# Kernel tuning notes

Measured on AMD Instinct MI355X. Metric: run time of the kernel, lower is better.

The kernel has to match this reference:

```python
import jax, jax.numpy as jnp
import numpy as np

LOSS_WEIGHT = 1.0


def setup_inputs() -> dict:
    key = jax.random.key(0)
    k1, k2 = jax.random.split(key)
    pred = jax.random.normal(k1, (4, 8192, 3), dtype=jnp.float32)
    target = jax.random.normal(k2, (4, 8192, 3), dtype=jnp.float32)
    return {"pred": pred, "target": target}


def _chamfer(pred, target):
    # pred: [B, N, 3], target: [B, M, 3]
    # squared pairwise distances d2[b, n, m] = ||pred[b,n] - target[b,m]||^2
    x2 = jnp.sum(pred * pred, axis=-1)            # [B, N]
    y2 = jnp.sum(target * target, axis=-1)        # [B, M]
    xy = jnp.einsum('bnd,bmd->bnm', pred, target)  # [B, N, M]
    d2 = x2[:, :, None] + y2[:, None, :] - 2.0 * xy
    d2 = jnp.maximum(d2, 0.0)  # numerical floor
    # bidirectional nearest-neighbor distances
    cham_x = jnp.min(d2, axis=2)  # [B, N] pred -> target
    cham_y = jnp.min(d2, axis=1)  # [B, M] target -> pred
    # point_reduction='mean' then batch_reduction='mean'
    loss = jnp.mean(cham_x, axis=1).mean() + jnp.mean(cham_y, axis=1).mean()
    return LOSS_WEIGHT * loss


def reference(pred, target):
    return _chamfer(pred, target)
```

## Files before the change

kernel.cpp:

```cpp
#include <hip/hip_runtime.h>

#define BATCH 4
#define NPTS 8192
#define PTOT (BATCH * NPTS)
#define NJH 8
#define TILES (NPTS / 32 / NJH)

typedef __attribute__((ext_vector_type(8))) short short8;
typedef __attribute__((ext_vector_type(16))) float f32x16;

__device__ __forceinline__ ushort f2bf(float f) {
    unsigned u = __float_as_uint(f);
    unsigned r = (u + 0x7fffu + ((u >> 16) & 1u)) >> 16;
    return (ushort)r;
}
__device__ __forceinline__ float bf2f(ushort b) {
    return __uint_as_float(((unsigned)b) << 16);
}

__device__ __forceinline__ float tree16(const f32x16 a, float run) {
    float m0 = fminf(fminf(a[0],  a[1]),  a[2]);
    float m1 = fminf(fminf(a[3],  a[4]),  a[5]);
    float m2 = fminf(fminf(a[6],  a[7]),  a[8]);
    float m3 = fminf(fminf(a[9],  a[10]), a[11]);
    float m4 = fminf(fminf(a[12], a[13]), a[14]);
    float n0 = fminf(fminf(m0, m1), m2);
    float n1 = fminf(fminf(m3, m4), a[15]);
    return fminf(run, fminf(n0, n1));
}

__global__ __launch_bounds__(256) void pack_k(const float* __restrict__ pred,
                                              const float* __restrict__ tgt,
                                              ushort* __restrict__ Qpan,
                                              ushort* __restrict__ Rpan) {
    int i = blockIdx.x * 256 + threadIdx.x;
    int cloud = (i >= PTOT) ? 1 : 0;
    int jg = cloud ? i - PTOT : i;
    const float* s = cloud ? tgt : pred;
    float c0 = s[3 * jg + 0], c1 = s[3 * jg + 1], c2 = s[3 * jg + 2];
    float c[3] = {c0, c1, c2};
    ushort hh[3], ll[3], mh[3], ml[3];
#pragma unroll
    for (int d = 0; d < 3; ++d) {
        ushort h = f2bf(c[d]); float hf = bf2f(h);
        ushort l = f2bf(c[d] - hf); float lf = bf2f(l);
        hh[d] = h; ll[d] = l;
        mh[d] = f2bf(-2.0f * hf);
        ml[d] = f2bf(-2.0f * lf);
    }
    float n2 = fmaf(c0, c0, fmaf(c1, c1, c2 * c2));
    ushort n2h = f2bf(n2);
    ushort n2l = f2bf(n2 - bf2f(n2h));
    const ushort ONE = 0x3F80;

    __attribute__((aligned(16))) ushort a[16] = {
        hh[0], hh[1], hh[2], ll[0], ll[1], ll[2], n2h, n2l,
        hh[0], hh[1], hh[2], ll[0], ll[1], ll[2], ONE, ONE};
    __attribute__((aligned(16))) ushort blo[8] = {
        mh[0], mh[1], mh[2], mh[0], mh[1], mh[2], ONE, ONE};
    __attribute__((aligned(16))) ushort bhi[8] = {
        ml[0], ml[1], ml[2], ml[0], ml[1], ml[2], n2h, n2l};

    ushort* ad = Qpan + (size_t)i * 16;
    *(uint4*)ad       = *(const uint4*)a;
    *(uint4*)(ad + 8) = *(const uint4*)(a + 8);

    int loc = jg & (NPTS - 1);
    int t   = loc >> 5;
    int col = loc & 31;
    size_t bb = ((size_t)cloud * PTOT + (size_t)(jg >> 13) * NPTS) * 16
              + (size_t)t * 512 + (size_t)col * 8;
    *(uint4*)(Rpan + bb)       = *(const uint4*)blo;
    *(uint4*)(Rpan + bb + 256) = *(const uint4*)bhi;
}

__global__ __launch_bounds__(512, 4) void chamfer_mfma_k(const ushort* __restrict__ Qpan,
                                                         const ushort* __restrict__ Rpan,
                                                         float* __restrict__ part) {
    __shared__ ushort Rsm[TILES * 512];

    int bid  = blockIdx.x;
    int qblk = bid & 15;
    int b    = (bid >> 4) & 3;
    int dir  = (bid >> 6) & 1;
    int jh   = bid >> 7;
    int tid  = threadIdx.x;
    int lane = tid & 63;
    int wave = tid >> 6;

    const ushort* Qp = Qpan + ((size_t)dir * PTOT + (size_t)b * NPTS) * 16;
    const ushort* Rp = Rpan + ((size_t)(1 - dir) * PTOT + (size_t)b * NPTS) * 16
                            + (size_t)jh * TILES * 512;

    {
        const float4* src = (const float4*)Rp;
        float4* dst = (float4*)Rsm;
#pragma unroll
        for (int it = 0; it < 4; ++it)
            dst[it * 512 + tid] = src[it * 512 + tid];
    }

    int q = qblk * 512 + wave * 64;
    const short8 qf0 = *reinterpret_cast<const short8*>(
        Qp + (size_t)(q + (lane & 31)) * 16 + 8 * (lane >> 5));
    const short8 qf1 = *reinterpret_cast<const short8*>(
        Qp + (size_t)(q + 32 + (lane & 31)) * 16 + 8 * (lane >> 5));

    __syncthreads();

    const ushort* rbase = Rsm + (size_t)(lane >> 5) * 256 + (size_t)(lane & 31) * 8;

    f32x16 zero = {};
    float run0 = 1e30f, run1 = 1e30f;

#pragma unroll 8
    for (int t = 0; t < TILES; ++t) {
        short8 r = *reinterpret_cast<const short8*>(rbase + (size_t)t * 512);
        f32x16 a0 = __builtin_amdgcn_mfma_f32_32x32x16_bf16(r, qf0, zero, 0, 0, 0);
        f32x16 a1 = __builtin_amdgcn_mfma_f32_32x32x16_bf16(r, qf1, zero, 0, 0, 0);
        run0 = tree16(a0, run0);
        run1 = tree16(a1, run1);
    }

    run0 = fminf(run0, __shfl_xor(run0, 32, 64));
    run1 = fminf(run1, __shfl_xor(run1, 32, 64));
    size_t pbase = (((size_t)jh * 2 + dir) * BATCH + b) * NPTS;
    part[pbase + q + lane] = (lane < 32) ? run0 : run1;
}

__global__ __launch_bounds__(256) void reduce1_k(const float* __restrict__ part,
                                                 float* __restrict__ bsum) {
    int q = blockIdx.x * 256 + threadIdx.x;
    float v = part[q];
#pragma unroll
    for (int jh = 1; jh < NJH; ++jh)
        v = fminf(v, part[(size_t)jh * 65536 + q]);
    v = fmaxf(v, 0.0f);
    for (int off = 32; off; off >>= 1) v += __shfl_down(v, off, 64);
    __shared__ float lds[4];
    int lane = threadIdx.x & 63, w = threadIdx.x >> 6;
    if (lane == 0) lds[w] = v;
    __syncthreads();
    if (threadIdx.x == 0)
        bsum[blockIdx.x] = (lds[0] + lds[1]) + (lds[2] + lds[3]);
}

__global__ __launch_bounds__(256) void reduce2_k(const float* __restrict__ bsum,
                                                 float* __restrict__ out) {
    float v = bsum[threadIdx.x];
    for (int off = 32; off; off >>= 1) v += __shfl_down(v, off, 64);
    __shared__ float lds[4];
    int lane = threadIdx.x & 63, w = threadIdx.x >> 6;
    if (lane == 0) lds[w] = v;
    __syncthreads();
    if (threadIdx.x == 0)
        out[0] = ((lds[0] + lds[1]) + (lds[2] + lds[3])) * (1.0f / 32768.0f);
}

extern "C" void kernel_launch(void* const* d_in, const int* in_sizes, int n_in,
                              void* d_out, int out_size, void* d_ws, size_t ws_size,
                              hipStream_t stream) {
    const float* pred = (const float*)d_in[0];
    const float* tgt  = (const float*)d_in[1];

    ushort* Qpan = (ushort*)d_ws;
    ushort* Rpan = Qpan + (size_t)2 * PTOT * 16;
    float*  part = (float*)(Rpan + (size_t)2 * PTOT * 16);
    float*  bsum = part + (size_t)NJH * 2 * PTOT;

    pack_k<<<(2 * PTOT) / 256, 256, 0, stream>>>(pred, tgt, Qpan, Rpan);
    chamfer_mfma_k<<<NJH * 2 * BATCH * 16, 512, 0, stream>>>(Qpan, Rpan, part);
    reduce1_k<<<256, 256, 0, stream>>>(part, bsum);
    reduce2_k<<<1, 256, 0, stream>>>(bsum, (float*)d_out);
}
```

Before: 31.17 us.

## Split target range finer, raise occupancy, add setprio, fuse final reductions

Doubles the number of target-range splits (NJH 8→16), giving 2048 blocks with half the LDS tile each, and raises the launch-bounds occupancy hint from 4 to 6. Wraps the MFMA loop in s_setprio and merges the two reduction kernels into one, using an atomic ticket counter that pack_k resets, so the last block does the final sum. The aim is better load balance and fewer launches. The cost is more partial-minimum traffic, since reduce now reads 16 slices, plus atomic and fence overhead.

```diff
diff --git a/kernel.cpp b/kernel.cpp
--- a/kernel.cpp
+++ b/kernel.cpp
@@ -3,7 +3,7 @@
 #define BATCH 4
 #define NPTS 8192
 #define PTOT (BATCH * NPTS)
-#define NJH 8
+#define NJH 16
 #define TILES (NPTS / 32 / NJH)
 
 typedef __attribute__((ext_vector_type(8))) short short8;
@@ -32,8 +32,10 @@
 __global__ __launch_bounds__(256) void pack_k(const float* __restrict__ pred,
                                               const float* __restrict__ tgt,
                                               ushort* __restrict__ Qpan,
-                                              ushort* __restrict__ Rpan) {
+                                              ushort* __restrict__ Rpan,
+                                              int* __restrict__ counter) {
     int i = blockIdx.x * 256 + threadIdx.x;
+    if (i == 0) *counter = 0;
     int cloud = (i >= PTOT) ? 1 : 0;
     int jg = cloud ? i - PTOT : i;
     const float* s = cloud ? tgt : pred;
@@ -74,7 +76,7 @@
     *(uint4*)(Rpan + bb + 256) = *(const uint4*)bhi;
 }
 
-__global__ __launch_bounds__(512, 4) void chamfer_mfma_k(const ushort* __restrict__ Qpan,
+__global__ __launch_bounds__(512, 6) void chamfer_mfma_k(const ushort* __restrict__ Qpan,
                                                          const ushort* __restrict__ Rpan,
                                                          float* __restrict__ part) {
     __shared__ ushort Rsm[TILES * 512];
@@ -95,9 +97,8 @@
     {
         const float4* src = (const float4*)Rp;
         float4* dst = (float4*)Rsm;
-#pragma unroll
-        for (int it = 0; it < 4; ++it)
-            dst[it * 512 + tid] = src[it * 512 + tid];
+        dst[tid]       = src[tid];
+        dst[512 + tid] = src[512 + tid];
     }
 
     int q = qblk * 512 + wave * 64;
@@ -113,6 +114,7 @@
     f32x16 zero = {};
     float run0 = 1e30f, run1 = 1e30f;
 
+    __builtin_amdgcn_s_setprio(1);
 #pragma unroll 8
     for (int t = 0; t < TILES; ++t) {
         short8 r = *reinterpret_cast<const short8*>(rbase + (size_t)t * 512);
@@ -121,6 +123,7 @@
         run0 = tree16(a0, run0);
         run1 = tree16(a1, run1);
     }
+    __builtin_amdgcn_s_setprio(0);
 
     run0 = fminf(run0, __shfl_xor(run0, 32, 64));
     run1 = fminf(run1, __shfl_xor(run1, 32, 64));
@@ -128,8 +131,10 @@
     part[pbase + q + lane] = (lane < 32) ? run0 : run1;
 }
 
-__global__ __launch_bounds__(256) void reduce1_k(const float* __restrict__ part,
-                                                 float* __restrict__ bsum) {
+__global__ __launch_bounds__(256) void reduce_k(const float* __restrict__ part,
+                                                float* __restrict__ bsum,
+                                                int* __restrict__ counter,
+                                                float* __restrict__ out) {
     int q = blockIdx.x * 256 + threadIdx.x;
     float v = part[q];
 #pragma unroll
@@ -138,23 +143,26 @@
     v = fmaxf(v, 0.0f);
     for (int off = 32; off; off >>= 1) v += __shfl_down(v, off, 64);
     __shared__ float lds[4];
+    __shared__ int ticket_s;
     int lane = threadIdx.x & 63, w = threadIdx.x >> 6;
     if (lane == 0) lds[w] = v;
     __syncthreads();
-    if (threadIdx.x == 0)
+    if (threadIdx.x == 0) {
         bsum[blockIdx.x] = (lds[0] + lds[1]) + (lds[2] + lds[3]);
-}
-
-__global__ __launch_bounds__(256) void reduce2_k(const float* __restrict__ bsum,
-                                                 float* __restrict__ out) {
-    float v = bsum[threadIdx.x];
-    for (int off = 32; off; off >>= 1) v += __shfl_down(v, off, 64);
-    __shared__ float lds[4];
-    int lane = threadIdx.x & 63, w = threadIdx.x >> 6;
-    if (lane == 0) lds[w] = v;
+        __threadfence();
+        ticket_s = atomicAdd(counter, 1);
+    }
     __syncthreads();
-    if (threadIdx.x == 0)
-        out[0] = ((lds[0] + lds[1]) + (lds[2] + lds[3])) * (1.0f / 32768.0f);
+    if (ticket_s == 255) {
+        __threadfence();
+        float s = bsum[threadIdx.x];
+        for (int off = 32; off; off >>= 1) s += __shfl_down(s, off, 64);
+        __syncthreads();
+        if (lane == 0) lds[w] = s;
+        __syncthreads();
+        if (threadIdx.x == 0)
+            out[0] = ((lds[0] + lds[1]) + (lds[2] + lds[3])) * (1.0f / 32768.0f);
+    }
 }
 
 extern "C" void kernel_launch(void* const* d_in, const int* in_sizes, int n_in,
@@ -167,9 +175,9 @@
     ushort* Rpan = Qpan + (size_t)2 * PTOT * 16;
     float*  part = (float*)(Rpan + (size_t)2 * PTOT * 16);
     float*  bsum = part + (size_t)NJH * 2 * PTOT;
+    int*    counter = (int*)(bsum + 256);
 
-    pack_k<<<(2 * PTOT) / 256, 256, 0, stream>>>(pred, tgt, Qpan, Rpan);
+    pack_k<<<(2 * PTOT) / 256, 256, 0, stream>>>(pred, tgt, Qpan, Rpan, counter);
     chamfer_mfma_k<<<NJH * 2 * BATCH * 16, 512, 0, stream>>>(Qpan, Rpan, part);
-    reduce1_k<<<256, 256, 0, stream>>>(part, bsum);
-    reduce2_k<<<1, 256, 0, stream>>>(bsum, (float*)d_out);
+    reduce_k<<<256, 256, 0, stream>>>(part, bsum, counter, (float*)d_out);
 }
```

Measured after the change: 38.01 us. +21.9%, slower.
